# Optimization experiments

Hardware: AMD Instinct MI355X
Metric: run time of the kernel (lower is better)

## Reference

```python
import jax, jax.numpy as jnp
import numpy as np

N = 30000      # nodes of type 'A'
IN = 128       # in_channels = hidden*2
H = 64         # hidden_channels
OUT = 64
M = 4          # number of metapaths (seq len for attention)
E = 480000     # edges per relation
NH = 8         # num_heads
HD = OUT // NH # head dim = 8
FF = 2048      # transformer dim_feedforward (torch default)
L = 2          # transformer layers
EPS = 1e-5


def setup_inputs() -> dict:
    key = jax.random.key(0)
    ks = iter(jax.random.split(key, 64))
    nk = lambda: next(ks)
    rn = lambda shape, s=0.05: (jax.random.normal(nk(), shape, jnp.float32) * s)
    x = jax.random.normal(nk(), (N, IN), jnp.float32)
    edge_index = jax.random.randint(nk(), (M, 2, E), 0, N, dtype=jnp.int32)
    counts = jnp.array([3.0, 1.0, 2.0, 2.0], jnp.float32)
    mp_weights = counts / counts.sum()
    inp = dict(x=x, edge_index=edge_index, mp_weights=mp_weights,
               W0=rn((M, H, IN)), b0=rn((M, H)), Wl=rn((M, H, IN)), bl=rn((M, H)),
               W1=rn((M, H, IN)), b1=rn((M, H)), Wo=rn((M, OUT, H)), bo=rn((M, OUT)),
               tinw=rn((L, 3 * OUT, OUT)), tinb=rn((L, 3 * OUT)),
               tow=rn((L, OUT, OUT)), tob=rn((L, OUT)),
               ln1g=jnp.ones((L, OUT)), ln1b=jnp.zeros((L, OUT)),
               ff1w=rn((L, FF, OUT)), ff1b=rn((L, FF)),
               ff2w=rn((L, OUT, FF)), ff2b=rn((L, OUT)),
               ln2g=jnp.ones((L, OUT)), ln2b=jnp.zeros((L, OUT)),
               r1w=rn((OUT, OUT)), r1b=rn((OUT,)), r2w=rn((1, OUT)), r2b=rn((1,)))
    return inp


def _layer_norm(v, g, b):
    mu = v.mean(-1, keepdims=True)
    var = ((v - mu) ** 2).mean(-1, keepdims=True)
    return (v - mu) / jnp.sqrt(var + EPS) * g + b


def reference(x, edge_index, mp_weights, W0, b0, Wl, bl, W1, b1, Wo, bo,
              tinw, tinb, tow, tob, ln1g, ln1b, ff1w, ff1b, ff2w, ff2b,
              ln2g, ln2b, r1w, r1b, r2w, r2b):
    n = x.shape[0]
    # ---- per-metapath GNN: gather + scatter-add + 3 fused linears ----
    embs = []
    for m in range(M):
        src, dst = edge_index[m, 0], edge_index[m, 1]
        # flow='target_to_source', aggr='add': agg[i] = sum_{e: src[e]==i} h[dst[e]]
        agg = jnp.zeros_like(x).at[src].add(x[dst])
        # w_l(agg) + w_0(h) + w_1(x), with h == x (forward passes x=h=h_dict[dst])
        h = jax.nn.relu(agg @ Wl[m].T + bl[m] + x @ (W0[m] + W1[m]).T + (b0[m] + b1[m]))
        embs.append(h @ Wo[m].T + bo[m])  # out_proj on updated start-type feats
    e = jnp.stack(embs, axis=1) * mp_weights[None, :, None]  # (N, M, OUT)

    # ---- 2-layer post-norm TransformerEncoder (batch_first, eval/no dropout) ----
    for l in range(L):
        qkv = e @ tinw[l].T + tinb[l]                       # (N, M, 3*OUT)
        q, k, v = jnp.split(qkv, 3, axis=-1)
        split = lambda t: t.reshape(n, M, NH, HD).transpose(0, 2, 1, 3)  # (N,NH,M,HD)
        q, k, v = split(q), split(k), split(v)
        attn = jax.nn.softmax(jnp.einsum('nhqd,nhkd->nhqk', q, k) / np.float32(np.sqrt(HD)), axis=-1)
        o = jnp.einsum('nhqk,nhkd->nhqd', attn, v).transpose(0, 2, 1, 3).reshape(n, M, OUT)
        o = o @ tow[l].T + tob[l]
        e = _layer_norm(e + o, ln1g[l], ln1b[l])
        f = jax.nn.relu(e @ ff1w[l].T + ff1b[l]) @ ff2w[l].T + ff2b[l]
        e = _layer_norm(e + f, ln2g[l], ln2b[l])

    pooled = e.mean(axis=1)                                  # (N, OUT)
    out = jax.nn.relu(pooled @ r1w.T + r1b) @ r2w.T + r2b    # (N, 1)
    return out[:, 0]
```

## Files before the change

### kernel.cpp

```cpp
#include <hip/hip_runtime.h>
#include <hip/hip_bf16.h>
#include <math.h>

#define N_NODES 30000
#define M_P     4
#define E_EDGES 480000
#define N_TOK   (N_NODES * 4)
#define N_ROWS  (M_P * N_NODES)
#define SLOTS   30
#define OVF_CAP 65536
#define LN_EPS  1e-5f

#define NB_FILL 1875
#define NB_LIN  3752

typedef short bf16x8 __attribute__((ext_vector_type(8)));
typedef float f32x4  __attribute__((ext_vector_type(4)));
#define MFMA_B16(a, b, c) __builtin_amdgcn_mfma_f32_16x16x32_bf16(a, b, c, 0, 0, 0)

__device__ inline unsigned short f2bf(float f) {
    union { float f; unsigned u; } v; v.f = f;
    unsigned r = v.u + 0x7fffu + ((v.u >> 16) & 1u);
    return (unsigned short)(r >> 16);
}
__device__ inline unsigned pack2bf(float a, float b) {
    union { __hip_bfloat162 h; unsigned u; } cv;
    cv.h = __float22bfloat162_rn(make_float2(a, b));
    return cv.u;
}
__device__ inline float bf2f(short s) {
    union { unsigned u; float f; } v; v.u = ((unsigned)(unsigned short)s) << 16;
    return v.f;
}
__device__ inline bf16x8 mk_frag(const float4& a, const float4& b) {
    union { uint4 u; bf16x8 v; } cv;
    cv.u = make_uint4(pack2bf(a.x, a.y), pack2bf(a.z, a.w),
                      pack2bf(b.x, b.y), pack2bf(b.z, b.w));
    return cv.v;
}

__global__ __launch_bounds__(256) void k_phaseA(
    const int* __restrict__ ei, unsigned short* __restrict__ bins,
    int* __restrict__ ovf_cnt, int2* __restrict__ ovf,
    const float* __restrict__ x,
    const float* __restrict__ Wl, const float* __restrict__ W0, const float* __restrict__ W1,
    const float* __restrict__ b0, const float* __restrict__ bl, const float* __restrict__ b1,
    unsigned short* __restrict__ ybf, unsigned short* __restrict__ zbf)
{
    __shared__ __align__(16) short Wf[8192];
    const int bid = blockIdx.x;
    const int t = threadIdx.x;

    if (bid < NB_FILL) {
        const int base = bid * 1024 + t;
        int rows[4], dsts[4];
        #pragma unroll
        for (int i = 0; i < 4; ++i) {
            const int g = base + i * 256;
            const int m = g / E_EDGES;
            const int e = g - m * E_EDGES;
            rows[i] = m * N_NODES + ei[(m * 2) * E_EDGES + e];
            dsts[i] = ei[(m * 2 + 1) * E_EDGES + e];
        }
        int pos[4];
        #pragma unroll
        for (int i = 0; i < 4; ++i)
            pos[i] = atomicAdd((int*)bins + rows[i] * 16, 1);
        #pragma unroll
        for (int i = 0; i < 4; ++i) {
            if (pos[i] < SLOTS) {
                bins[rows[i] * 32 + 2 + pos[i]] = (unsigned short)dsts[i];
            } else {
                const int ix = atomicAdd(ovf_cnt, 1);
                if (ix < OVF_CAP) ovf[ix] = make_int2(rows[i], dsts[i]);
            }
        }
    } else {
        const int lid = bid - NB_FILL;
        const int bx = lid % 469;
        const int by = lid / 469;
        const int which = by >> 2, m = by & 3;
        const int w = t >> 6, lane = t & 63;
        const int m_ = lane & 15, qc = lane >> 4;
        const int node = bx * 64 + w * 16 + m_;

        #pragma unroll
        for (int i = 0; i < 32; ++i) {
            const int d = t + 256 * i;
            const int fg = d >> 9, rem = d & 511;
            const int qmm = rem >> 3, j = d & 7;
            const int q = qmm >> 4, mm = qmm & 15;
            const int ot = fg >> 2, hh = fg & 3;
            const int row = ot * 16 + mm, k = hh * 32 + q * 8 + j;
            float v;
            if (which == 0) v = Wl[(m * 64 + row) * 128 + k];
            else            v = W0[(m * 64 + row) * 128 + k] + W1[(m * 64 + row) * 128 + k];
            Wf[d] = (short)f2bf(v);
        }

        bf16x8 xb[4];
        #pragma unroll
        for (int hh = 0; hh < 4; ++hh) {
            float4 a = make_float4(0.f, 0.f, 0.f, 0.f), b = a;
            if (node < N_NODES) {
                a = *(const float4*)(x + node * 128 + hh * 32 + qc * 8);
                b = *(const float4*)(x + node * 128 + hh * 32 + qc * 8 + 4);
            }
            xb[hh] = mk_frag(a, b);
        }
        __syncthreads();

        f32x4 acc[4];
        #pragma unroll
        for (int ot = 0; ot < 4; ++ot) {
            f32x4 c = {};
            if (which) {
                const int o = m * 64 + ot * 16 + qc * 4;
                const float4 v0 = *(const float4*)(b0 + o);
                const float4 v1 = *(const float4*)(b1 + o);
                const float4 vl = *(const float4*)(bl + o);
                c[0] = v0.x + v1.x + vl.x; c[1] = v0.y + v1.y + vl.y;
                c[2] = v0.z + v1.z + vl.z; c[3] = v0.w + v1.w + vl.w;
            }
            #pragma unroll
            for (int hh = 0; hh < 4; ++hh) {
                const bf16x8 wa = *(const bf16x8*)&Wf[(ot * 4 + hh) * 512 + lane * 8];
                c = MFMA_B16(wa, xb[hh], c);
            }
            acc[ot] = c;
        }
        unsigned short* outp = which ? zbf : ybf;
        if (node < N_NODES) {
            #pragma unroll
            for (int ot = 0; ot < 4; ++ot) {
                uint2 pk = make_uint2(pack2bf(acc[ot][0], acc[ot][1]),
                                      pack2bf(acc[ot][2], acc[ot][3]));
                *(uint2*)(outp + ((size_t)m * N_NODES + node) * 64 + ot * 16 + qc * 4) = pk;
            }
        }
    }
}

__global__ __launch_bounds__(256) void k_gather(
    const unsigned short* __restrict__ bins,
    const int* __restrict__ ovf_cnt, const int2* __restrict__ ovf,
    const unsigned short* __restrict__ ybf, float* __restrict__ aggh)
{
    const int w = threadIdx.x >> 6, lane = threadIdx.x & 63;
    const int row = blockIdx.x * 4 + w;
    const int m = row / N_NODES;
    const unsigned short* ym = ybf + (size_t)m * N_NODES * 64;
    const int v = (lane < 32) ? bins[row * 32 + lane] : 0;
    const int v0 = __shfl(v, 0), v1 = __shfl(v, 1);
    const int tot = (v0 & 0xffff) | (v1 << 16);
    const int cnt = min(tot, SLOTS);
    float a0 = 0.f, a1 = 0.f, a2 = 0.f, a3 = 0.f;
    int j = 0;
    for (; j + 4 <= cnt; j += 4) {
        const int r0 = __shfl(v, j + 2), r1 = __shfl(v, j + 3);
        const int r2 = __shfl(v, j + 4), r3 = __shfl(v, j + 5);
        a0 += bf2f((short)ym[r0 * 64 + lane]); a1 += bf2f((short)ym[r1 * 64 + lane]);
        a2 += bf2f((short)ym[r2 * 64 + lane]); a3 += bf2f((short)ym[r3 * 64 + lane]);
    }
    for (; j < cnt; ++j) {
        const int r = __shfl(v, j + 2);
        a0 += bf2f((short)ym[r * 64 + lane]);
    }
    if (tot > SLOTS) {
        const int no = min(*ovf_cnt, OVF_CAP);
        for (int i2 = 0; i2 < no; ++i2) {
            const int2 ent = ovf[i2];
            if (ent.x == row) a0 += bf2f((short)ym[ent.y * 64 + lane]);
        }
    }
    aggh[(size_t)row * 64 + lane] = (a0 + a1) + (a2 + a3);
}

__global__ __launch_bounds__(256) void k_emb_ws(
    const float* __restrict__ aggh, const unsigned short* __restrict__ zbf,
    const float* __restrict__ Wo, const float* __restrict__ bo,
    const float* __restrict__ mpw, float* __restrict__ e,
    const float* __restrict__ ff1w, const float* __restrict__ ff2w,
    const float* __restrict__ tinw, const float* __restrict__ tow,
    unsigned short* __restrict__ w1s, unsigned short* __restrict__ w2s,
    unsigned short* __restrict__ wqkv_s, unsigned short* __restrict__ tow_s)
{
    __shared__ float hT[64][20];
    __shared__ float WoT[64][64];
    const int t = threadIdx.x;
    const int bid = blockIdx.x;

    if (bid >= N_NODES / 16) {
        const int g = (bid - N_NODES / 16) * 256 + t;
        {
            const int l = g >> 17, r2 = g & 131071;
            const int f = r2 >> 6, k = r2 & 63;
            const int c = f >> 6, fc = f & 63, ft = fc >> 4, m = fc & 15;
            const int h = k >> 5, q = (k >> 3) & 3, j = k & 7;
            w1s[l * 131072 + c * 4096 + (ft * 2 + h) * 512 + (q * 16 + m) * 8 + j] = f2bf(ff1w[g]);
        }
        {
            const int l = g >> 17, r2 = g & 131071;
            const int o = r2 >> 11, f = r2 & 2047;
            const int c = f >> 6, fc = f & 63, h = fc >> 5, q = (fc >> 3) & 3, j = fc & 7;
            const int ot = o >> 4, m = o & 15;
            w2s[l * 131072 + c * 4096 + (ot * 2 + h) * 512 + (q * 16 + m) * 8 + j] = f2bf(ff2w[g]);
        }
        if (g < 2 * 192 * 64) {
            const int l = g / 12288, r2 = g - l * 12288;
            const int f = r2 >> 6, k = r2 & 63;
            const int ft = f >> 4, m = f & 15;
            const int h = k >> 5, q = (k >> 3) & 3, j = k & 7;
            wqkv_s[l * 12288 + (ft * 2 + h) * 512 + (q * 16 + m) * 8 + j] = f2bf(tinw[g]);
        }
        if (g < 2 * 64 * 64) {
            const int l = g >> 12, r2 = g & 4095;
            const int o = r2 >> 6, k = r2 & 63;
            const int ot = o >> 4, m = o & 15;
            const int h = k >> 5, q = (k >> 3) & 3, j = k & 7;
            tow_s[l * 4096 + (ot * 2 + h) * 512 + (q * 16 + m) * 8 + j] = f2bf(tow[g]);
        }
        return;
    }

    const int node0 = bid * 16;
    for (int m = 0; m < 4; ++m) {
        #pragma unroll
        for (int i = 0; i < 4; ++i) {
            const int o  = (t & 15) + 16 * i;
            const int kq = t >> 4;
            const float4 v = *(const float4*)(Wo + (m * 64 + o) * 64 + kq * 4);
            WoT[kq * 4 + 0][o] = v.x; WoT[kq * 4 + 1][o] = v.y;
            WoT[kq * 4 + 2][o] = v.z; WoT[kq * 4 + 3][o] = v.w;
        }
        {
            const int node = t & 15, kq = t >> 4;
            const int n = node0 + node;
            const float4 a = *(const float4*)(aggh + ((size_t)m * N_NODES + n) * 64 + kq * 4);
            const uint2 bz = *(const uint2*)(zbf + ((size_t)m * N_NODES + n) * 64 + kq * 4);
            hT[kq * 4 + 0][node] = fmaxf(a.x + bf2f((short)(bz.x & 0xffff)), 0.f);
            hT[kq * 4 + 1][node] = fmaxf(a.y + bf2f((short)(bz.x >> 16)), 0.f);
            hT[kq * 4 + 2][node] = fmaxf(a.z + bf2f((short)(bz.y & 0xffff)), 0.f);
            hT[kq * 4 + 3][node] = fmaxf(a.w + bf2f((short)(bz.y >> 16)), 0.f);
        }
        __syncthreads();
        const int o = t & 63, nl4 = (t >> 6) * 4;
        float acc[4] = {};
        #pragma unroll 8
        for (int k = 0; k < 64; ++k) {
            const float bw = WoT[k][o];
            const float4 a = *(const float4*)&hT[k][nl4];
            acc[0] += a.x * bw; acc[1] += a.y * bw; acc[2] += a.z * bw; acc[3] += a.w * bw;
        }
        const float bb = bo[m * 64 + o];
        const float w  = mpw[m];
        #pragma unroll
        for (int i = 0; i < 4; ++i)
            e[((node0 + nl4 + i) * 4 + m) * 64 + o] = (acc[i] + bb) * w;
        __syncthreads();
    }
}

__global__ __launch_bounds__(256, 3) void k_attn_mfma(
    const float* __restrict__ e,
    const unsigned short* __restrict__ wqkv_s, const float* __restrict__ tinb,
    const unsigned short* __restrict__ tow_s, const float* __restrict__ tob,
    const float* __restrict__ ln1g, const float* __restrict__ ln1b,
    float* __restrict__ eout, int l)
{
    __shared__ __align__(16) short QK[17408];
    __shared__ __align__(16) short Vb[9216];
    const int t = threadIdx.x;
    const int w = t >> 6, lane = t & 63;
    const int m_ = lane & 15, qc = lane >> 4;
    const int tok0 = blockIdx.x * 128;
    short* QKw = &QK[w * 4352];
    short* Vw  = &Vb[w * 2304];

    bf16x8 xb[2][2];
    #pragma unroll
    for (int nt = 0; nt < 2; ++nt)
        #pragma unroll
        for (int h = 0; h < 2; ++h) {
            const int tok = tok0 + w * 32 + nt * 16 + m_;
            const int k0 = h * 32 + qc * 8;
            float4 a = make_float4(0.f, 0.f, 0.f, 0.f), b = a;
            if (tok < N_TOK) {
                a = *(const float4*)(e + tok * 64 + k0);
                b = *(const float4*)(e + tok * 64 + k0 + 4);
            }
            xb[nt][h] = mk_frag(a, b);
        }

    const unsigned short* Wq = wqkv_s + l * 12288;
    f32x4 acc[12][2];
    #pragma unroll
    for (int ft = 0; ft < 12; ++ft) {
        const bf16x8 wa0 = *(const bf16x8*)(Wq + (ft * 2 + 0) * 512 + lane * 8);
        const bf16x8 wa1 = *(const bf16x8*)(Wq + (ft * 2 + 1) * 512 + lane * 8);
        const float4 bv = *(const float4*)(tinb + l * 192 + ft * 16 + qc * 4);
        f32x4 c0; c0[0] = bv.x; c0[1] = bv.y; c0[2] = bv.z; c0[3] = bv.w;
        f32x4 c1 = c0;
        c0 = MFMA_B16(wa0, xb[0][0], c0); c0 = MFMA_B16(wa1, xb[0][1], c0);
        c1 = MFMA_B16(wa0, xb[1][0], c1); c1 = MFMA_B16(wa1, xb[1][1], c1);
        acc[ft][0] = c0; acc[ft][1] = c1;
    }
    #pragma unroll
    for (int ft = 0; ft < 8; ++ft)
        #pragma unroll
        for (int nt = 0; nt < 2; ++nt) {
            const int addr = (nt * 16 + m_) * 136 + ft * 16 + qc * 4;
            *(uint2*)&QKw[addr] = make_uint2(pack2bf(acc[ft][nt][0], acc[ft][nt][1]),
                                             pack2bf(acc[ft][nt][2], acc[ft][nt][3]));
        }
    #pragma unroll
    for (int ft = 8; ft < 12; ++ft)
        #pragma unroll
        for (int nt = 0; nt < 2; ++nt) {
            const int addr = (nt * 16 + m_) * 72 + (ft - 8) * 16 + qc * 4;
            *(uint2*)&Vw[addr] = make_uint2(pack2bf(acc[ft][nt][0], acc[ft][nt][1]),
                                            pack2bf(acc[ft][nt][2], acc[ft][nt][3]));
        }

    {
        const int node = lane >> 3, head = lane & 7;
        float kk[4][8], vv[4][8], qv[4][8];
        #pragma unroll
        for (int j2 = 0; j2 < 4; ++j2) {
            const bf16x8 kr = *(const bf16x8*)&QKw[(node * 4 + j2) * 136 + 64 + head * 8];
            const bf16x8 vr = *(const bf16x8*)&Vw[(node * 4 + j2) * 72 + head * 8];
            const bf16x8 qr = *(const bf16x8*)&QKw[(node * 4 + j2) * 136 + head * 8];
            #pragma unroll
            for (int d = 0; d < 8; ++d) {
                kk[j2][d] = bf2f(kr[d]); vv[j2][d] = bf2f(vr[d]); qv[j2][d] = bf2f(qr[d]);
            }
        }
        const float scale = 0.35355339059327373f;
        const int nt2 = node >> 2, hq = head >> 2, qq = head & 3;
        #pragma unroll
        for (int i = 0; i < 4; ++i) {
            float s[4];
            #pragma unroll
            for (int j2 = 0; j2 < 4; ++j2) {
                float a2 = 0.f;
                #pragma unroll
                for (int d = 0; d < 8; ++d) a2 += qv[i][d] * kk[j2][d];
                s[j2] = a2 * scale;
            }
            const float mx = fmaxf(fmaxf(s[0], s[1]), fmaxf(s[2], s[3]));
            float p[4], sum = 0.f;
            #pragma unroll
            for (int j2 = 0; j2 < 4; ++j2) { p[j2] = __expf(s[j2] - mx); sum += p[j2]; }
            const float inv = 1.f / sum;
            float o[8];
            #pragma unroll
            for (int d = 0; d < 8; ++d)
                o[d] = (p[0] * vv[0][d] + p[1] * vv[1][d] + p[2] * vv[2][d] + p[3] * vv[3][d]) * inv;
            const int n = (node & 3) * 4 + i;
            *(uint4*)&QKw[(nt2 * 2 + hq) * 512 + qq * 128 + n * 8] =
                make_uint4(pack2bf(o[0], o[1]), pack2bf(o[2], o[3]),
                           pack2bf(o[4], o[5]), pack2bf(o[6], o[7]));
        }
    }

    bf16x8 ob[2][2];
    #pragma unroll
    for (int nt = 0; nt < 2; ++nt)
        #pragma unroll
        for (int h = 0; h < 2; ++h)
            ob[nt][h] = *(const bf16x8*)&QKw[(nt * 2 + h) * 512 + lane * 8];
    const unsigned short* Tw = tow_s + l * 4096;
    f32x4 acc2[4][2] = {};
    #pragma unroll
    for (int ot = 0; ot < 4; ++ot) {
        const bf16x8 t0 = *(const bf16x8*)(Tw + (ot * 2 + 0) * 512 + lane * 8);
        const bf16x8 t1 = *(const bf16x8*)(Tw + (ot * 2 + 1) * 512 + lane * 8);
        acc2[ot][0] = MFMA_B16(t0, ob[0][0], acc2[ot][0]);
        acc2[ot][0] = MFMA_B16(t1, ob[0][1], acc2[ot][0]);
        acc2[ot][1] = MFMA_B16(t0, ob[1][0], acc2[ot][1]);
        acc2[ot][1] = MFMA_B16(t1, ob[1][1], acc2[ot][1]);
    }

    float4 tbv[4], gv[4], bv2[4];
    #pragma unroll
    for (int ot = 0; ot < 4; ++ot) {
        const int o = l * 64 + ot * 16 + qc * 4;
        tbv[ot] = *(const float4*)(tob + o);
        gv[ot]  = *(const float4*)(ln1g + o);
        bv2[ot] = *(const float4*)(ln1b + o);
    }
    #pragma unroll
    for (int nt = 0; nt < 2; ++nt) {
        const int tok = tok0 + w * 32 + nt * 16 + m_;
        const bool valid = tok < N_TOK;
        float v[4][4];
        float s = 0.f;
        #pragma unroll
        for (int ot = 0; ot < 4; ++ot) {
            float4 rs = make_float4(0.f, 0.f, 0.f, 0.f);
            if (valid) rs = *(const float4*)(e + tok * 64 + ot * 16 + qc * 4);
            v[ot][0] = acc2[ot][nt][0] + tbv[ot].x + rs.x;
            v[ot][1] = acc2[ot][nt][1] + tbv[ot].y + rs.y;
            v[ot][2] = acc2[ot][nt][2] + tbv[ot].z + rs.z;
            v[ot][3] = acc2[ot][nt][3] + tbv[ot].w + rs.w;
            s += v[ot][0] + v[ot][1] + v[ot][2] + v[ot][3];
        }
        s += __shfl_xor(s, 16); s += __shfl_xor(s, 32);
        const float mean = s * (1.f / 64.f);
        float vs = 0.f;
        #pragma unroll
        for (int ot = 0; ot < 4; ++ot)
            #pragma unroll
            for (int r = 0; r < 4; ++r) { v[ot][r] -= mean; vs += v[ot][r] * v[ot][r]; }
        vs += __shfl_xor(vs, 16); vs += __shfl_xor(vs, 32);
        const float rr = rsqrtf(vs * (1.f / 64.f) + LN_EPS);
        if (valid) {
            #pragma unroll
            for (int ot = 0; ot < 4; ++ot) {
                float4 o4 = make_float4(v[ot][0] * rr * gv[ot].x + bv2[ot].x,
                                        v[ot][1] * rr * gv[ot].y + bv2[ot].y,
                                        v[ot][2] * rr * gv[ot].z + bv2[ot].z,
                                        v[ot][3] * rr * gv[ot].w + bv2[ot].w);
                *(float4*)(eout + tok * 64 + ot * 16 + qc * 4) = o4;
            }
        }
    }
}

__global__ __launch_bounds__(256, 4) void k_ffn_mfma(
    const float* __restrict__ e,
    const unsigned short* __restrict__ w1s, const unsigned short* __restrict__ w2s,
    const float* __restrict__ ff1b, const float* __restrict__ ff2b,
    const float* __restrict__ ln2g, const float* __restrict__ ln2b,
    float* __restrict__ eout, int l)
{
    __shared__ __align__(16) short Act[8192];
    __shared__ __align__(16) short Wb[8192];
    const int t = threadIdx.x;
    const int w = t >> 6, lane = t & 63;
    const int m_ = lane & 15, qc = lane >> 4;
    const int tok0 = blockIdx.x * 128;
    short* Aw = &Act[w * 2048];

    bf16x8 xb[2][2];
    #pragma unroll
    for (int nt = 0; nt < 2; ++nt)
        #pragma unroll
        for (int h = 0; h < 2; ++h) {
            const int tok = tok0 + w * 32 + nt * 16 + m_;
            const int k0 = h * 32 + qc * 8;
            float4 a = make_float4(0.f, 0.f, 0.f, 0.f), b = a;
            if (tok < N_TOK) {
                a = *(const float4*)(e + tok * 64 + k0);
                b = *(const float4*)(e + tok * 64 + k0 + 4);
            }
            xb[nt][h] = mk_frag(a, b);
        }

    const uint4* gw1 = (const uint4*)(w1s + l * 131072);
    const uint4* gw2 = (const uint4*)(w2s + l * 131072);
    uint4 p0 = gw1[t], p1 = gw1[t + 256], p2 = gw2[t], p3 = gw2[t + 256];
    *(uint4*)&Wb[t * 8] = p0;            *(uint4*)&Wb[(t + 256) * 8] = p1;
    *(uint4*)&Wb[4096 + t * 8] = p2;     *(uint4*)&Wb[4096 + (t + 256) * 8] = p3;

    f32x4 acc[4][2] = {};

    for (int c = 0; c < 32; ++c) {
        __syncthreads();
        if (c < 31) {
            p0 = gw1[(c + 1) * 512 + t];       p1 = gw1[(c + 1) * 512 + t + 256];
            p2 = gw2[(c + 1) * 512 + t];       p3 = gw2[(c + 1) * 512 + t + 256];
        }
        #pragma unroll
        for (int ft = 0; ft < 4; ++ft) {
            const bf16x8 wa0 = *(const bf16x8*)&Wb[(ft * 2 + 0) * 512 + lane * 8];
            const bf16x8 wa1 = *(const bf16x8*)&Wb[(ft * 2 + 1) * 512 + lane * 8];
            const float4 bv = *(const float4*)(ff1b + l * 2048 + c * 64 + ft * 16 + qc * 4);
            f32x4 c0; c0[0] = bv.x; c0[1] = bv.y; c0[2] = bv.z; c0[3] = bv.w;
            f32x4 c1 = c0;
            c0 = MFMA_B16(wa0, xb[0][0], c0); c0 = MFMA_B16(wa1, xb[0][1], c0);
            c1 = MFMA_B16(wa0, xb[1][0], c1); c1 = MFMA_B16(wa1, xb[1][1], c1);
            const int ha = ft >> 1, qa = (ft & 1) * 2 + (qc >> 1), jo = (qc & 1) * 4;
            const int boff = ha * 512 + qa * 128 + m_ * 8 + jo;
            *(uint2*)&Aw[boff] =
                make_uint2(pack2bf(fmaxf(c0[0], 0.f), fmaxf(c0[1], 0.f)),
                           pack2bf(fmaxf(c0[2], 0.f), fmaxf(c0[3], 0.f)));
            *(uint2*)&Aw[boff + 1024] =
                make_uint2(pack2bf(fmaxf(c1[0], 0.f), fmaxf(c1[1], 0.f)),
                           pack2bf(fmaxf(c1[2], 0.f), fmaxf(c1[3], 0.f)));
        }
        bf16x8 ab[2][2];
        #pragma unroll
        for (int nt = 0; nt < 2; ++nt)
            #pragma unroll
            for (int h = 0; h < 2; ++h)
                ab[nt][h] = *(const bf16x8*)&Aw[(nt * 2 + h) * 512 + lane * 8];
        #pragma unroll
        for (int ot = 0; ot < 4; ++ot) {
            const bf16x8 w20 = *(const bf16x8*)&Wb[4096 + (ot * 2 + 0) * 512 + lane * 8];
            const bf16x8 w21 = *(const bf16x8*)&Wb[4096 + (ot * 2 + 1) * 512 + lane * 8];
            acc[ot][0] = MFMA_B16(w20, ab[0][0], acc[ot][0]);
            acc[ot][0] = MFMA_B16(w21, ab[0][1], acc[ot][0]);
            acc[ot][1] = MFMA_B16(w20, ab[1][0], acc[ot][1]);
            acc[ot][1] = MFMA_B16(w21, ab[1][1], acc[ot][1]);
        }
        __syncthreads();
        if (c < 31) {
            *(uint4*)&Wb[t * 8] = p0;            *(uint4*)&Wb[(t + 256) * 8] = p1;
            *(uint4*)&Wb[4096 + t * 8] = p2;     *(uint4*)&Wb[4096 + (t + 256) * 8] = p3;
        }
    }

    float4 fb2v[4], gv[4], bv2[4];
    #pragma unroll
    for (int ot = 0; ot < 4; ++ot) {
        const int o = l * 64 + ot * 16 + qc * 4;
        fb2v[ot] = *(const float4*)(ff2b + o);
        gv[ot]   = *(const float4*)(ln2g + o);
        bv2[ot]  = *(const float4*)(ln2b + o);
    }
    #pragma unroll
    for (int nt = 0; nt < 2; ++nt) {
        const int tok = tok0 + w * 32 + nt * 16 + m_;
        const bool valid = tok < N_TOK;
        float v[4][4];
        float s = 0.f;
        #pragma unroll
        for (int ot = 0; ot < 4; ++ot) {
            float4 rs = make_float4(0.f, 0.f, 0.f, 0.f);
            if (valid) rs = *(const float4*)(e + tok * 64 + ot * 16 + qc * 4);
            v[ot][0] = acc[ot][nt][0] + fb2v[ot].x + rs.x;
            v[ot][1] = acc[ot][nt][1] + fb2v[ot].y + rs.y;
            v[ot][2] = acc[ot][nt][2] + fb2v[ot].z + rs.z;
            v[ot][3] = acc[ot][nt][3] + fb2v[ot].w + rs.w;
            s += v[ot][0] + v[ot][1] + v[ot][2] + v[ot][3];
        }
        s += __shfl_xor(s, 16); s += __shfl_xor(s, 32);
        const float mean = s * (1.f / 64.f);
        float vs = 0.f;
        #pragma unroll
        for (int ot = 0; ot < 4; ++ot)
            #pragma unroll
            for (int r = 0; r < 4; ++r) { v[ot][r] -= mean; vs += v[ot][r] * v[ot][r]; }
        vs += __shfl_xor(vs, 16); vs += __shfl_xor(vs, 32);
        const float rr = rsqrtf(vs * (1.f / 64.f) + LN_EPS);
        if (valid) {
            #pragma unroll
            for (int ot = 0; ot < 4; ++ot) {
                float4 o4 = make_float4(v[ot][0] * rr * gv[ot].x + bv2[ot].x,
                                        v[ot][1] * rr * gv[ot].y + bv2[ot].y,
                                        v[ot][2] * rr * gv[ot].z + bv2[ot].z,
                                        v[ot][3] * rr * gv[ot].w + bv2[ot].w);
                *(float4*)(eout + tok * 64 + ot * 16 + qc * 4) = o4;
            }
        }
    }
}

__global__ __launch_bounds__(256) void k_reg(
    const float* __restrict__ e,
    const float* __restrict__ r1w, const float* __restrict__ r1b,
    const float* __restrict__ r2w, const float* __restrict__ r2b,
    float* __restrict__ out)
{
    __shared__ float r1T[64][64];
    __shared__ float pld[4][64];
    const int t = threadIdx.x;
    #pragma unroll
    for (int i = 0; i < 4; ++i) {
        const int j  = (t & 15) + 16 * i;
        const int kq = t >> 4;
        const float4 v = *(const float4*)(r1w + j * 64 + kq * 4);
        r1T[kq * 4 + 0][j] = v.x; r1T[kq * 4 + 1][j] = v.y;
        r1T[kq * 4 + 2][j] = v.z; r1T[kq * 4 + 3][j] = v.w;
    }
    const int w = t >> 6, lane = t & 63;
    const int n = blockIdx.x * 4 + w;
    const float p = 0.25f * (e[(n * 4 + 0) * 64 + lane] + e[(n * 4 + 1) * 64 + lane] +
                             e[(n * 4 + 2) * 64 + lane] + e[(n * 4 + 3) * 64 + lane]);
    pld[w][lane] = p;
    __syncthreads();
    float acc = r1b[lane];
    #pragma unroll 8
    for (int k = 0; k < 64; ++k) acc += pld[w][k] * r1T[k][lane];
    acc = fmaxf(acc, 0.f);
    float partial = acc * r2w[lane];
    partial += __shfl_xor(partial, 1);  partial += __shfl_xor(partial, 2);
    partial += __shfl_xor(partial, 4);  partial += __shfl_xor(partial, 8);
    partial += __shfl_xor(partial, 16); partial += __shfl_xor(partial, 32);
    if (lane == 0) out[n] = partial + r2b[0];
}

extern "C" void kernel_launch(void* const* d_in, const int* in_sizes, int n_in,
                              void* d_out, int out_size, void* d_ws, size_t ws_size,
                              hipStream_t stream) {
    const float* x    = (const float*)d_in[0];
    const int*   ei   = (const int*)d_in[1];
    const float* mpw  = (const float*)d_in[2];
    const float* W0   = (const float*)d_in[3];
    const float* b0   = (const float*)d_in[4];
    const float* Wl   = (const float*)d_in[5];
    const float* bl   = (const float*)d_in[6];
    const float* W1   = (const float*)d_in[7];
    const float* b1   = (const float*)d_in[8];
    const float* Wo   = (const float*)d_in[9];
    const float* bo   = (const float*)d_in[10];
    const float* tinw = (const float*)d_in[11];
    const float* tinb = (const float*)d_in[12];
    const float* tow  = (const float*)d_in[13];
    const float* tob  = (const float*)d_in[14];
    const float* ln1g = (const float*)d_in[15];
    const float* ln1b = (const float*)d_in[16];
    const float* ff1w = (const float*)d_in[17];
    const float* ff1b = (const float*)d_in[18];
    const float* ff2w = (const float*)d_in[19];
    const float* ff2b = (const float*)d_in[20];
    const float* ln2g = (const float*)d_in[21];
    const float* ln2b = (const float*)d_in[22];
    const float* r1w  = (const float*)d_in[23];
    const float* r1b  = (const float*)d_in[24];
    const float* r2w  = (const float*)d_in[25];
    const float* r2b  = (const float*)d_in[26];

    const size_t CH = (size_t)M_P * N_NODES * 64;
    float* y    = (float*)d_ws;
    float* zz   = y + CH;
    float* aggh = zz + CH;
    float* e    = aggh + CH;
    unsigned short* ybf = (unsigned short*)y;
    unsigned short* zbf = (unsigned short*)zz;
    unsigned short* w1s    = (unsigned short*)y;
    unsigned short* w2s    = w1s + 262144;
    unsigned short* wqkv_s = w2s + 262144;
    unsigned short* tow_s  = wqkv_s + 24576;
    unsigned short* bins = (unsigned short*)e;
    int* ovf_cnt = (int*)((char*)e + (size_t)N_ROWS * 64);
    int2* ovf    = (int2*)((char*)ovf_cnt + 16);

    hipMemsetAsync(bins, 0, (size_t)N_ROWS * 64 + 16, stream);
    k_phaseA<<<NB_FILL + NB_LIN, 256, 0, stream>>>(ei, bins, ovf_cnt, ovf,
                                                   x, Wl, W0, W1, b0, bl, b1, ybf, zbf);
    k_gather<<<N_ROWS / 4, 256, 0, stream>>>(bins, ovf_cnt, ovf, ybf, aggh);
    k_emb_ws<<<N_NODES / 16 + 1024, 256, 0, stream>>>(aggh, zbf, Wo, bo, mpw, e,
                                                      ff1w, ff2w, tinw, tow,
                                                      w1s, w2s, wqkv_s, tow_s);
    for (int l = 0; l < 2; ++l) {
        k_attn_mfma<<<(N_TOK + 127) / 128, 256, 0, stream>>>(e, wqkv_s, tinb, tow_s, tob,
                                                             ln1g, ln1b, e, l);
        k_ffn_mfma<<<(N_TOK + 127) / 128, 256, 0, stream>>>(e, w1s, w2s, ff1b, ff2b,
                                                            ln2g, ln2b, e, l);
    }
    k_reg<<<N_NODES / 4, 256, 0, stream>>>(e, r1w, r1b, r2w, r2b, (float*)d_out);
}
```

Before: 573.6 us.

## Fuse attention and FFN sublayers into one per-layer transformer kernel

Merges the attention+LN1 kernel and the FFN+LN2 kernel into a single k_layer kernel per transformer layer. The post-LN1 activations stay in registers as the FFN residual and go to the FFN input fragments through shared memory, instead of a global write followed by a global read. This removes one launch and one round trip of the activation tensor through global memory per layer. In exchange it adds register pressure and a larger shared-memory union, which may lower occupancy (launch bounds stay at 3 where the FFN kernel had 4).

```diff
diff --git a/kernel.cpp b/kernel.cpp
--- a/kernel.cpp
+++ b/kernel.cpp
@@ -261,21 +261,23 @@
     }
 }
 
-__global__ __launch_bounds__(256, 3) void k_attn_mfma(
+__global__ __launch_bounds__(256, 3) void k_layer(
     const float* __restrict__ e,
     const unsigned short* __restrict__ wqkv_s, const float* __restrict__ tinb,
     const unsigned short* __restrict__ tow_s, const float* __restrict__ tob,
     const float* __restrict__ ln1g, const float* __restrict__ ln1b,
+    const unsigned short* __restrict__ w1s, const unsigned short* __restrict__ w2s,
+    const float* __restrict__ ff1b, const float* __restrict__ ff2b,
+    const float* __restrict__ ln2g, const float* __restrict__ ln2b,
     float* __restrict__ eout, int l)
 {
-    __shared__ __align__(16) short QK[17408];
-    __shared__ __align__(16) short Vb[9216];
+    __shared__ __align__(16) short U[26624];
     const int t = threadIdx.x;
     const int w = t >> 6, lane = t & 63;
     const int m_ = lane & 15, qc = lane >> 4;
     const int tok0 = blockIdx.x * 128;
-    short* QKw = &QK[w * 4352];
-    short* Vw  = &Vb[w * 2304];
+    short* QKw = &U[w * 4352];
+    short* Vw  = &U[17408 + w * 2304];
 
     bf16x8 xb[2][2];
     #pragma unroll
@@ -293,34 +295,36 @@
         }
 
     const unsigned short* Wq = wqkv_s + l * 12288;
-    f32x4 acc[12][2];
-    #pragma unroll
-    for (int ft = 0; ft < 12; ++ft) {
-        const bf16x8 wa0 = *(const bf16x8*)(Wq + (ft * 2 + 0) * 512 + lane * 8);
-        const bf16x8 wa1 = *(const bf16x8*)(Wq + (ft * 2 + 1) * 512 + lane * 8);
-        const float4 bv = *(const float4*)(tinb + l * 192 + ft * 16 + qc * 4);
-        f32x4 c0; c0[0] = bv.x; c0[1] = bv.y; c0[2] = bv.z; c0[3] = bv.w;
-        f32x4 c1 = c0;
-        c0 = MFMA_B16(wa0, xb[0][0], c0); c0 = MFMA_B16(wa1, xb[0][1], c0);
-        c1 = MFMA_B16(wa0, xb[1][0], c1); c1 = MFMA_B16(wa1, xb[1][1], c1);
-        acc[ft][0] = c0; acc[ft][1] = c1;
-    }
-    #pragma unroll
-    for (int ft = 0; ft < 8; ++ft)
-        #pragma unroll
-        for (int nt = 0; nt < 2; ++nt) {
-            const int addr = (nt * 16 + m_) * 136 + ft * 16 + qc * 4;
-            *(uint2*)&QKw[addr] = make_uint2(pack2bf(acc[ft][nt][0], acc[ft][nt][1]),
-                                             pack2bf(acc[ft][nt][2], acc[ft][nt][3]));
-        }
-    #pragma unroll
-    for (int ft = 8; ft < 12; ++ft)
-        #pragma unroll
-        for (int nt = 0; nt < 2; ++nt) {
-            const int addr = (nt * 16 + m_) * 72 + (ft - 8) * 16 + qc * 4;
-            *(uint2*)&Vw[addr] = make_uint2(pack2bf(acc[ft][nt][0], acc[ft][nt][1]),
-                                            pack2bf(acc[ft][nt][2], acc[ft][nt][3]));
-        }
+    {
+        f32x4 acc[12][2];
+        #pragma unroll
+        for (int ft = 0; ft < 12; ++ft) {
+            const bf16x8 wa0 = *(const bf16x8*)(Wq + (ft * 2 + 0) * 512 + lane * 8);
+            const bf16x8 wa1 = *(const bf16x8*)(Wq + (ft * 2 + 1) * 512 + lane * 8);
+            const float4 bv = *(const float4*)(tinb + l * 192 + ft * 16 + qc * 4);
+            f32x4 c0; c0[0] = bv.x; c0[1] = bv.y; c0[2] = bv.z; c0[3] = bv.w;
+            f32x4 c1 = c0;
+            c0 = MFMA_B16(wa0, xb[0][0], c0); c0 = MFMA_B16(wa1, xb[0][1], c0);
+            c1 = MFMA_B16(wa0, xb[1][0], c1); c1 = MFMA_B16(wa1, xb[1][1], c1);
+            acc[ft][0] = c0; acc[ft][1] = c1;
+        }
+        #pragma unroll
+        for (int ft = 0; ft < 8; ++ft)
+            #pragma unroll
+            for (int nt = 0; nt < 2; ++nt) {
+                const int addr = (nt * 16 + m_) * 136 + ft * 16 + qc * 4;
+                *(uint2*)&QKw[addr] = make_uint2(pack2bf(acc[ft][nt][0], acc[ft][nt][1]),
+                                                 pack2bf(acc[ft][nt][2], acc[ft][nt][3]));
+            }
+        #pragma unroll
+        for (int ft = 8; ft < 12; ++ft)
+            #pragma unroll
+            for (int nt = 0; nt < 2; ++nt) {
+                const int addr = (nt * 16 + m_) * 72 + (ft - 8) * 16 + qc * 4;
+                *(uint2*)&Vw[addr] = make_uint2(pack2bf(acc[ft][nt][0], acc[ft][nt][1]),
+                                                pack2bf(acc[ft][nt][2], acc[ft][nt][3]));
+            }
+    }
 
     {
         const int node = lane >> 3, head = lane & 7;
@@ -381,81 +385,70 @@
         acc2[ot][1] = MFMA_B16(t1, ob[1][1], acc2[ot][1]);
     }
 
-    float4 tbv[4], gv[4], bv2[4];
-    #pragma unroll
-    for (int ot = 0; ot < 4; ++ot) {
-        const int o = l * 64 + ot * 16 + qc * 4;
-        tbv[ot] = *(const float4*)(tob + o);
-        gv[ot]  = *(const float4*)(ln1g + o);
-        bv2[ot] = *(const float4*)(ln1b + o);
-    }
-    #pragma unroll
-    for (int nt = 0; nt < 2; ++nt) {
-        const int tok = tok0 + w * 32 + nt * 16 + m_;
-        const bool valid = tok < N_TOK;
-        float v[4][4];
-        float s = 0.f;
+    float resid[2][4][4];
+    {
+        float4 tbv[4], gv[4], bv2[4];
         #pragma unroll
         for (int ot = 0; ot < 4; ++ot) {
-            float4 rs = make_float4(0.f, 0.f, 0.f, 0.f);
-            if (valid) rs = *(const float4*)(e + tok * 64 + ot * 16 + qc * 4);
-            v[ot][0] = acc2[ot][nt][0] + tbv[ot].x + rs.x;
-            v[ot][1] = acc2[ot][nt][1] + tbv[ot].y + rs.y;
-            v[ot][2] = acc2[ot][nt][2] + tbv[ot].z + rs.z;
-            v[ot][3] = acc2[ot][nt][3] + tbv[ot].w + rs.w;
-            s += v[ot][0] + v[ot][1] + v[ot][2] + v[ot][3];
-        }
-        s += __shfl_xor(s, 16); s += __shfl_xor(s, 32);
-        const float mean = s * (1.f / 64.f);
-        float vs = 0.f;
-        #pragma unroll
-        for (int ot = 0; ot < 4; ++ot)
-            #pragma unroll
-            for (int r = 0; r < 4; ++r) { v[ot][r] -= mean; vs += v[ot][r] * v[ot][r]; }
-        vs += __shfl_xor(vs, 16); vs += __shfl_xor(vs, 32);
-        const float rr = rsqrtf(vs * (1.f / 64.f) + LN_EPS);
-        if (valid) {
+            const int o = l * 64 + ot * 16 + qc * 4;
+            tbv[ot] = *(const float4*)(tob + o);
+            gv[ot]  = *(const float4*)(ln1g + o);
+            bv2[ot] = *(const float4*)(ln1b + o);
+        }
+        #pragma unroll
+        for (int nt = 0; nt < 2; ++nt) {
+            const int tok = tok0 + w * 32 + nt * 16 + m_;
+            const bool valid = tok < N_TOK;
+            float v[4][4];
+            float s = 0.f;
             #pragma unroll
             for (int ot = 0; ot < 4; ++ot) {
-                float4 o4 = make_float4(v[ot][0] * rr * gv[ot].x + bv2[ot].x,
-                                        v[ot][1] * rr * gv[ot].y + bv2[ot].y,
-                                        v[ot][2] * rr * gv[ot].z + bv2[ot].z,
-                                        v[ot][3] * rr * gv[ot].w + bv2[ot].w);
-                *(float4*)(eout + tok * 64 + ot * 16 + qc * 4) = o4;
-            }
-        }
-    }
-}
-
-__global__ __launch_bounds__(256, 4) void k_ffn_mfma(
-    const float* __restrict__ e,
-    const unsigned short* __restrict__ w1s, const unsigned short* __restrict__ w2s,
-    const float* __restrict__ ff1b, const float* __restrict__ ff2b,
-    const float* __restrict__ ln2g, const float* __restrict__ ln2b,
-    float* __restrict__ eout, int l)
-{
-    __shared__ __align__(16) short Act[8192];
-    __shared__ __align__(16) short Wb[8192];
-    const int t = threadIdx.x;
-    const int w = t >> 6, lane = t & 63;
-    const int m_ = lane & 15, qc = lane >> 4;
-    const int tok0 = blockIdx.x * 128;
-    short* Aw = &Act[w * 2048];
-
-    bf16x8 xb[2][2];
+                float4 rs = make_float4(0.f, 0.f, 0.f, 0.f);
+                if (valid) rs = *(const float4*)(e + tok * 64 + ot * 16 + qc * 4);
+                v[ot][0] = acc2[ot][nt][0] + tbv[ot].x + rs.x;
+                v[ot][1] = acc2[ot][nt][1] + tbv[ot].y + rs.y;
+                v[ot][2] = acc2[ot][nt][2] + tbv[ot].z + rs.z;
+                v[ot][3] = acc2[ot][nt][3] + tbv[ot].w + rs.w;
+                s += v[ot][0] + v[ot][1] + v[ot][2] + v[ot][3];
+            }
+            s += __shfl_xor(s, 16); s += __shfl_xor(s, 32);
+            const float mean = s * (1.f / 64.f);
+            float vs = 0.f;
+            #pragma unroll
+            for (int ot = 0; ot < 4; ++ot)
+                #pragma unroll
+                for (int r = 0; r < 4; ++r) { v[ot][r] -= mean; vs += v[ot][r] * v[ot][r]; }
+            vs += __shfl_xor(vs, 16); vs += __shfl_xor(vs, 32);
+            const float rr = rsqrtf(vs * (1.f / 64.f) + LN_EPS);
+            #pragma unroll
+            for (int ot = 0; ot < 4; ++ot) {
+                resid[nt][ot][0] = v[ot][0] * rr * gv[ot].x + bv2[ot].x;
+                resid[nt][ot][1] = v[ot][1] * rr * gv[ot].y + bv2[ot].y;
+                resid[nt][ot][2] = v[ot][2] * rr * gv[ot].z + bv2[ot].z;
+                resid[nt][ot][3] = v[ot][3] * rr * gv[ot].w + bv2[ot].w;
+            }
+        }
+    }
+
+    __syncthreads();
+    short* Wb = U;
+    short* Aw = &U[8192 + w * 2048];
+
     #pragma unroll
     for (int nt = 0; nt < 2; ++nt)
         #pragma unroll
-        for (int h = 0; h < 2; ++h) {
-            const int tok = tok0 + w * 32 + nt * 16 + m_;
-            const int k0 = h * 32 + qc * 8;
-            float4 a = make_float4(0.f, 0.f, 0.f, 0.f), b = a;
-            if (tok < N_TOK) {
-                a = *(const float4*)(e + tok * 64 + k0);
-                b = *(const float4*)(e + tok * 64 + k0 + 4);
-            }
-            xb[nt][h] = mk_frag(a, b);
-        }
+        for (int ot = 0; ot < 4; ++ot) {
+            const int ha = ot >> 1, qa = (ot & 1) * 2 + (qc >> 1), jo = (qc & 1) * 4;
+            *(uint2*)&Aw[(nt * 2 + ha) * 512 + qa * 128 + m_ * 8 + jo] =
+                make_uint2(pack2bf(resid[nt][ot][0], resid[nt][ot][1]),
+                           pack2bf(resid[nt][ot][2], resid[nt][ot][3]));
+        }
+    bf16x8 xb2[2][2];
+    #pragma unroll
+    for (int nt = 0; nt < 2; ++nt)
+        #pragma unroll
+        for (int h = 0; h < 2; ++h)
+            xb2[nt][h] = *(const bf16x8*)&Aw[(nt * 2 + h) * 512 + lane * 8];
 
     const uint4* gw1 = (const uint4*)(w1s + l * 131072);
     const uint4* gw2 = (const uint4*)(w2s + l * 131072);
@@ -478,8 +471,8 @@
             const float4 bv = *(const float4*)(ff1b + l * 2048 + c * 64 + ft * 16 + qc * 4);
             f32x4 c0; c0[0] = bv.x; c0[1] = bv.y; c0[2] = bv.z; c0[3] = bv.w;
             f32x4 c1 = c0;
-            c0 = MFMA_B16(wa0, xb[0][0], c0); c0 = MFMA_B16(wa1, xb[0][1], c0);
-            c1 = MFMA_B16(wa0, xb[1][0], c1); c1 = MFMA_B16(wa1, xb[1][1], c1);
+            c0 = MFMA_B16(wa0, xb2[0][0], c0); c0 = MFMA_B16(wa1, xb2[0][1], c0);
+            c1 = MFMA_B16(wa0, xb2[1][0], c1); c1 = MFMA_B16(wa1, xb2[1][1], c1);
             const int ha = ft >> 1, qa = (ft & 1) * 2 + (qc >> 1), jo = (qc & 1) * 4;
             const int boff = ha * 512 + qa * 128 + m_ * 8 + jo;
             *(uint2*)&Aw[boff] =
@@ -527,12 +520,10 @@
         float s = 0.f;
         #pragma unroll
         for (int ot = 0; ot < 4; ++ot) {
-            float4 rs = make_float4(0.f, 0.f, 0.f, 0.f);
-            if (valid) rs = *(const float4*)(e + tok * 64 + ot * 16 + qc * 4);
-            v[ot][0] = acc[ot][nt][0] + fb2v[ot].x + rs.x;
-            v[ot][1] = acc[ot][nt][1] + fb2v[ot].y + rs.y;
-            v[ot][2] = acc[ot][nt][2] + fb2v[ot].z + rs.z;
-            v[ot][3] = acc[ot][nt][3] + fb2v[ot].w + rs.w;
+            v[ot][0] = acc[ot][nt][0] + fb2v[ot].x + resid[nt][ot][0];
+            v[ot][1] = acc[ot][nt][1] + fb2v[ot].y + resid[nt][ot][1];
+            v[ot][2] = acc[ot][nt][2] + fb2v[ot].z + resid[nt][ot][2];
+            v[ot][3] = acc[ot][nt][3] + fb2v[ot].w + resid[nt][ot][3];
             s += v[ot][0] + v[ot][1] + v[ot][2] + v[ot][3];
         }
         s += __shfl_xor(s, 16); s += __shfl_xor(s, 32);
@@ -645,10 +636,9 @@
                                                       ff1w, ff2w, tinw, tow,
                                                       w1s, w2s, wqkv_s, tow_s);
     for (int l = 0; l < 2; ++l) {
-        k_attn_mfma<<<(N_TOK + 127) / 128, 256, 0, stream>>>(e, wqkv_s, tinb, tow_s, tob,
-                                                             ln1g, ln1b, e, l);
-        k_ffn_mfma<<<(N_TOK + 127) / 128, 256, 0, stream>>>(e, w1s, w2s, ff1b, ff2b,
-                                                            ln2g, ln2b, e, l);
+        k_layer<<<(N_TOK + 127) / 128, 256, 0, stream>>>(e, wqkv_s, tinb, tow_s, tob,
+                                                         ln1g, ln1b, w1s, w2s, ff1b, ff2b,
+                                                         ln2g, ln2b, e, l);
     }
     k_reg<<<N_NODES / 4, 256, 0, stream>>>(e, r1w, r1b, r2w, r2b, (float*)d_out);
 }
```

After: 578.5 us. Within noise of the previous version (+0.9%).
